# Optimization experiments

Measured on AMD Instinct MI355X. Metric: run time of the kernel, lower is better.

The kernel has to match this reference:

```python
import jax, jax.numpy as jnp
import numpy as np

D_MODEL = 512
N_HEADS = 8
D_HEAD = D_MODEL // N_HEADS


def setup_inputs() -> dict:
    key = jax.random.key(0)
    ks = jax.random.split(key, 10)
    B, N = 4, 2048
    s = 1.0 / np.sqrt(D_MODEL)
    inp = {
        'x': jax.random.normal(ks[0], (B, N, D_MODEL), jnp.float32),
        'attn_bias': jax.random.normal(ks[1], (B, 1, N, N), jnp.float32),
        'wq': jax.random.normal(ks[2], (D_MODEL, D_MODEL), jnp.float32) * s,
        'bq': jnp.zeros((D_MODEL,), jnp.float32),
        'wk': jax.random.normal(ks[3], (D_MODEL, D_MODEL), jnp.float32) * s,
        'bk': jnp.zeros((D_MODEL,), jnp.float32),
        'wv': jax.random.normal(ks[4], (D_MODEL, D_MODEL), jnp.float32) * s,
        'bv': jnp.zeros((D_MODEL,), jnp.float32),
        'wo': jax.random.normal(ks[5], (D_MODEL, D_MODEL), jnp.float32) * s,
        'bo': jnp.zeros((D_MODEL,), jnp.float32),
    }
    return inp


def reference(x, attn_bias, wq, bq, wk, bk, wv, bv, wo, bo):
    B, N, D = x.shape
    h, dh = N_HEADS, D_HEAD
    # projections; weights stored as (in, out) so y = x @ w + b
    q = (x @ wq + bq).reshape(B, N, h, dh).transpose(0, 2, 1, 3)  # (B,h,N,dh)
    k = (x @ wk + bk).reshape(B, N, h, dh).transpose(0, 2, 1, 3)
    v = (x @ wv + bv).reshape(B, N, h, dh).transpose(0, 2, 1, 3)
    scores = jnp.einsum('bhnd,bhmd->bhnm', q, k) / jnp.sqrt(jnp.float32(dh))
    scores = scores + attn_bias  # broadcast over heads
    attn = jax.nn.softmax(scores, axis=-1)
    out = jnp.einsum('bhnm,bhmd->bhnd', attn, v)
    out = out.transpose(0, 2, 1, 3).reshape(B, N, D)
    return out @ wo + bo
```

## Files before the change

kernel.cpp:

```cpp
#include <hip/hip_runtime.h>
#include <hip/hip_bf16.h>

typedef __bf16 bf16x8 __attribute__((ext_vector_type(8)));
typedef float f32x4 __attribute__((ext_vector_type(4)));
typedef float f32x16 __attribute__((ext_vector_type(16)));
using u16 = unsigned short;
using u32 = unsigned int;

#define LDSS 72

__device__ __forceinline__ u16 f2bf(float f) {
  union { float f; u32 u; } v; v.f = f;
  u32 r = v.u + 0x7fffu + ((v.u >> 16) & 1u);
  return (u16)(r >> 16);
}

__device__ __forceinline__ u32 cvt_pk_bf16(float lo, float hi) {
  u32 r;
  asm("v_cvt_pk_bf16_f32 %0, %1, %2" : "=v"(r) : "v"(lo), "v"(hi));
  return r;
}

__global__ void cast_x_kernel(const float* __restrict__ x, u16* __restrict__ xb) {
  int i = (blockIdx.x * 256 + threadIdx.x) * 8;
  float4 f0 = *(const float4*)&x[i];
  float4 f1 = *(const float4*)&x[i + 4];
  u16 u[8];
  u[0] = f2bf(f0.x); u[1] = f2bf(f0.y); u[2] = f2bf(f0.z); u[3] = f2bf(f0.w);
  u[4] = f2bf(f1.x); u[5] = f2bf(f1.y); u[6] = f2bf(f1.z); u[7] = f2bf(f1.w);
  *(uint4*)&xb[i] = *(uint4*)u;
}

__global__ __launch_bounds__(256) void cast_wT_kernel(
    const float* __restrict__ w0, const float* __restrict__ w1,
    const float* __restrict__ w2, const float* __restrict__ w3,
    u16* __restrict__ t0, u16* __restrict__ t1,
    u16* __restrict__ t2, u16* __restrict__ t3) {
  __shared__ u16 tl[64][72];
  int wi = blockIdx.z;
  const float* w; u16* t;
  if (wi == 0)      { w = w0; t = t0; }
  else if (wi == 1) { w = w1; t = t1; }
  else if (wi == 2) { w = w2; t = t2; }
  else              { w = w3; t = t3; }
  int r0 = blockIdx.x * 64, c0 = blockIdx.y * 64;
  int tid = threadIdx.x;
  int row = tid >> 2, q = tid & 3;
#pragma unroll
  for (int j = 0; j < 4; j++) {
    float4 f = *(const float4*)&w[(r0 + row) * 512 + c0 + q * 16 + j * 4];
    tl[row][q * 16 + j * 4 + 0] = f2bf(f.x);
    tl[row][q * 16 + j * 4 + 1] = f2bf(f.y);
    tl[row][q * 16 + j * 4 + 2] = f2bf(f.z);
    tl[row][q * 16 + j * 4 + 3] = f2bf(f.w);
  }
  __syncthreads();
  int crow = tid >> 2;
  u16 tmp[16];
#pragma unroll
  for (int j = 0; j < 16; j++) tmp[j] = tl[q * 16 + j][crow];
  *(uint4*)&t[(c0 + crow) * 512 + r0 + q * 16]     = *(uint4*)&tmp[0];
  *(uint4*)&t[(c0 + crow) * 512 + r0 + q * 16 + 8] = *(uint4*)&tmp[8];
}

__global__ __launch_bounds__(256) void proj_kernel(
    const u16* __restrict__ xb,
    const u16* __restrict__ wqT, const u16* __restrict__ wkT, const u16* __restrict__ wvT,
    const float* __restrict__ bq, const float* __restrict__ bk, const float* __restrict__ bv,
    u16* __restrict__ Q, u16* __restrict__ K, u16* __restrict__ Vt) {
  __shared__ u16 Alds[64 * LDSS];
  __shared__ u16 Blds[64 * LDSS];
  int which = blockIdx.z;
  const u16* wT; const float* bias; u16* out;
  if (which == 0)      { wT = wqT; bias = bq; out = Q; }
  else if (which == 1) { wT = wkT; bias = bk; out = K; }
  else                 { wT = wvT; bias = bv; out = Vt; }

  int m0 = blockIdx.y * 64;
  int n0 = blockIdx.x * 64;
  int tid = threadIdx.x;
  int lane = tid & 63, w = tid >> 6;
  int wm = w >> 1, wn = w & 1;
  int l15 = lane & 15, l4 = lane >> 4;

  int r0 = tid >> 3, c8 = (tid & 7) * 8;

  uint4 ar0 = *(const uint4*)&xb[(m0 + r0) * 512 + c8];
  uint4 ar1 = *(const uint4*)&xb[(m0 + r0 + 32) * 512 + c8];
  uint4 br0 = *(const uint4*)&wT[(n0 + r0) * 512 + c8];
  uint4 br1 = *(const uint4*)&wT[(n0 + r0 + 32) * 512 + c8];

  f32x4 acc[2][2] = {};
  for (int ks = 0; ks < 8; ks++) {
    __syncthreads();
    *(uint4*)&Alds[r0 * LDSS + c8]        = ar0;
    *(uint4*)&Alds[(r0 + 32) * LDSS + c8] = ar1;
    *(uint4*)&Blds[r0 * LDSS + c8]        = br0;
    *(uint4*)&Blds[(r0 + 32) * LDSS + c8] = br1;
    __syncthreads();
    if (ks < 7) {
      int k0 = (ks + 1) * 64;
      ar0 = *(const uint4*)&xb[(m0 + r0) * 512 + k0 + c8];
      ar1 = *(const uint4*)&xb[(m0 + r0 + 32) * 512 + k0 + c8];
      br0 = *(const uint4*)&wT[(n0 + r0) * 512 + k0 + c8];
      br1 = *(const uint4*)&wT[(n0 + r0 + 32) * 512 + k0 + c8];
    }
#pragma unroll
    for (int kk = 0; kk < 2; kk++) {
      bf16x8 a[2], b[2];
#pragma unroll
      for (int f = 0; f < 2; f++) {
        a[f] = *(const bf16x8*)&Alds[(wm * 32 + f * 16 + l15) * LDSS + kk * 32 + l4 * 8];
        b[f] = *(const bf16x8*)&Blds[(wn * 32 + f * 16 + l15) * LDSS + kk * 32 + l4 * 8];
      }
#pragma unroll
      for (int fm = 0; fm < 2; fm++)
#pragma unroll
        for (int fn = 0; fn < 2; fn++) {
          if (which == 2)
            acc[fm][fn] = __builtin_amdgcn_mfma_f32_16x16x32_bf16(b[fn], a[fm], acc[fm][fn], 0, 0, 0);
          else
            acc[fm][fn] = __builtin_amdgcn_mfma_f32_16x16x32_bf16(a[fm], b[fn], acc[fm][fn], 0, 0, 0);
        }
    }
  }
  int bidx = m0 >> 11;
  int head = n0 >> 6;
  if (which == 2) {
#pragma unroll
    for (int fm = 0; fm < 2; fm++)
#pragma unroll
      for (int fn = 0; fn < 2; fn++)
#pragma unroll
        for (int r = 0; r < 4; r++) {
          int drow = wn * 32 + fn * 16 + l4 * 4 + r;
          int col  = wm * 32 + fm * 16 + l15;
          float vv = acc[fm][fn][r] + bias[n0 + drow];
          out[((size_t)(bidx * 8 + head) * 64 + drow) * 2048 + (m0 & 2047) + col] = f2bf(vv);
        }
  } else {
#pragma unroll
    for (int fm = 0; fm < 2; fm++)
#pragma unroll
      for (int fn = 0; fn < 2; fn++)
#pragma unroll
        for (int r = 0; r < 4; r++) {
          int row = wm * 32 + fm * 16 + l4 * 4 + r;
          int col = wn * 32 + fn * 16 + l15;
          int nrow = (m0 & 2047) + row;
          float vv = acc[fm][fn][r] + bias[n0 + col];
          out[(((size_t)(bidx * 8 + head) * 2048) + nrow) * 64 + col] = f2bf(vv);
        }
  }
}

__global__ __launch_bounds__(256, 2) void attn_kernel(
    const u16* __restrict__ Q, const u16* __restrict__ K, const u16* __restrict__ Vt,
    const float* __restrict__ bias, u16* __restrict__ O) {
  __shared__ u16 Klds[64 * LDSS];
  __shared__ u16 Vtlds[64 * LDSS];

  int qt = blockIdx.x, h = blockIdx.y, b = blockIdx.z;
  int tid = threadIdx.x;
  int lane = tid & 63, w = tid >> 6;
  int l31 = lane & 31, hi = lane >> 5;
  int qrow = qt * 128 + w * 32 + l31;

  const u16* Qbh  = Q  + (size_t)(b * 8 + h) * 2048 * 64;
  const u16* Kbh  = K  + (size_t)(b * 8 + h) * 2048 * 64;
  const u16* Vtbh = Vt + (size_t)(b * 8 + h) * 64 * 2048;
  const float* biasq = bias + (size_t)b * 2048 * 2048 + (size_t)qrow * 2048;

  bf16x8 qf[4];
#pragma unroll
  for (int dk = 0; dk < 4; dk++)
    qf[dk] = *(const bf16x8*)&Qbh[qrow * 64 + dk * 16 + hi * 8];

  f32x16 o[2] = {};
  float mrow = -1e30f, lrow = 0.f;

  int r0 = tid >> 3, c8 = (tid & 7) * 8;

  uint4 kr0 = *(const uint4*)&Kbh[r0 * 64 + c8];
  uint4 kr1 = *(const uint4*)&Kbh[(32 + r0) * 64 + c8];
  uint4 vr0 = *(const uint4*)&Vtbh[r0 * 2048 + c8];
  uint4 vr1 = *(const uint4*)&Vtbh[(r0 + 32) * 2048 + c8];
  float4 bb[8];
#pragma unroll
  for (int kt = 0; kt < 2; kt++)
#pragma unroll
    for (int g = 0; g < 4; g++)
      bb[kt * 4 + g] = *(const float4*)&biasq[kt * 32 + 8 * g + 4 * hi];

  for (int t = 0; t < 32; t++) {
    __syncthreads();
    *(uint4*)&Klds[r0 * LDSS + c8]         = kr0;
    *(uint4*)&Klds[(r0 + 32) * LDSS + c8]  = kr1;
    *(uint4*)&Vtlds[r0 * LDSS + c8]        = vr0;
    *(uint4*)&Vtlds[(r0 + 32) * LDSS + c8] = vr1;
    __syncthreads();

    bool pf = (t < 31);
    if (pf) {
      kr0 = *(const uint4*)&Kbh[((t + 1) * 64 + r0) * 64 + c8];
      kr1 = *(const uint4*)&Kbh[((t + 1) * 64 + 32 + r0) * 64 + c8];
      vr0 = *(const uint4*)&Vtbh[r0 * 2048 + (t + 1) * 64 + c8];
      vr1 = *(const uint4*)&Vtbh[(r0 + 32) * 2048 + (t + 1) * 64 + c8];
    }

    f32x16 s[2] = {};
    __builtin_amdgcn_s_setprio(1);
#pragma unroll
    for (int dk = 0; dk < 4; dk++) {
      bf16x8 a0 = *(const bf16x8*)&Klds[l31 * LDSS + dk * 16 + hi * 8];
      s[0] = __builtin_amdgcn_mfma_f32_32x32x16_bf16(a0, qf[dk], s[0], 0, 0, 0);
      bf16x8 a1 = *(const bf16x8*)&Klds[(32 + l31) * LDSS + dk * 16 + hi * 8];
      s[1] = __builtin_amdgcn_mfma_f32_32x32x16_bf16(a1, qf[dk], s[1], 0, 0, 0);
    }
    __builtin_amdgcn_s_setprio(0);

    float m = -1e30f;
#pragma unroll
    for (int kt = 0; kt < 2; kt++)
#pragma unroll
      for (int g = 0; g < 4; g++) {
        float4 bv4 = bb[kt * 4 + g];
#pragma unroll
        for (int j = 0; j < 4; j++) {
          float val = s[kt][g * 4 + j] * 0.125f + ((const float*)&bv4)[j];
          s[kt][g * 4 + j] = val;
          m = fmaxf(m, val);
        }
      }
    m = fmaxf(m, __shfl_xor(m, 32));

    if (!__all(m <= mrow + 8.0f)) {
      float mnew = fmaxf(mrow, m);
      float corr = __expf(mrow - mnew);
      mrow = mnew;
      lrow *= corr;
#pragma unroll
      for (int dt = 0; dt < 2; dt++)
#pragma unroll
        for (int i = 0; i < 16; i++) o[dt][i] *= corr;
    }

    u32 c[2][8];
    float sum = 0.f;
#pragma unroll
    for (int kt = 0; kt < 2; kt++)
#pragma unroll
      for (int g = 0; g < 4; g++) {
        float p0 = __expf(s[kt][g * 4 + 0] - mrow);
        float p1 = __expf(s[kt][g * 4 + 1] - mrow);
        float p2 = __expf(s[kt][g * 4 + 2] - mrow);
        float p3 = __expf(s[kt][g * 4 + 3] - mrow);
        sum += (p0 + p1) + (p2 + p3);
        c[kt][2 * g]     = cvt_pk_bf16(p0, p1);
        c[kt][2 * g + 1] = cvt_pk_bf16(p2, p3);
      }
    sum += __shfl_xor(sum, 32);
    lrow += sum;

    u32 dx[2][8];
#pragma unroll
    for (int kt = 0; kt < 2; kt++)
#pragma unroll
      for (int j = 0; j < 8; j++)
        dx[kt][j] = (u32)__shfl_xor((int)c[kt][j], 32);

    if (pf) {
#pragma unroll
      for (int kt = 0; kt < 2; kt++)
#pragma unroll
        for (int g = 0; g < 4; g++)
          bb[kt * 4 + g] = *(const float4*)&biasq[(t + 1) * 64 + kt * 32 + 8 * g + 4 * hi];
    }

    __builtin_amdgcn_s_setprio(1);
#pragma unroll
    for (int kk = 0; kk < 4; kk++) {
      const int kt = kk >> 1, jA = 4 * (kk & 1);
      union { u32 u[4]; bf16x8 v; } pfg;
      pfg.u[0] = hi ? dx[kt][jA + 2] : c[kt][jA];
      pfg.u[1] = hi ? dx[kt][jA + 3] : c[kt][jA + 1];
      pfg.u[2] = hi ? c[kt][jA + 2]  : dx[kt][jA];
      pfg.u[3] = hi ? c[kt][jA + 3]  : dx[kt][jA + 1];
#pragma unroll
      for (int dt = 0; dt < 2; dt++) {
        bf16x8 va = *(const bf16x8*)&Vtlds[(dt * 32 + l31) * LDSS + kk * 16 + hi * 8];
        o[dt] = __builtin_amdgcn_mfma_f32_32x32x16_bf16(va, pfg.v, o[dt], 0, 0, 0);
      }
    }
    __builtin_amdgcn_s_setprio(0);
  }

  float inv = 1.0f / lrow;
  size_t obase = (size_t)(b * 2048 + qrow) * 512 + h * 64;
#pragma unroll
  for (int dt = 0; dt < 2; dt++)
#pragma unroll
    for (int g = 0; g < 4; g++) {
      uint2 pr;
      pr.x = cvt_pk_bf16(o[dt][4 * g + 0] * inv, o[dt][4 * g + 1] * inv);
      pr.y = cvt_pk_bf16(o[dt][4 * g + 2] * inv, o[dt][4 * g + 3] * inv);
      *(uint2*)&O[obase + dt * 32 + 8 * g + 4 * hi] = pr;
    }
}

__global__ __launch_bounds__(256) void outproj_kernel(
    const u16* __restrict__ Ob, const u16* __restrict__ woT,
    const float* __restrict__ bo, float* __restrict__ out) {
  __shared__ u16 Alds[64 * LDSS];
  __shared__ u16 Blds[64 * LDSS];
  int m0 = blockIdx.y * 64;
  int n0 = blockIdx.x * 64;
  int tid = threadIdx.x;
  int lane = tid & 63, w = tid >> 6;
  int wm = w >> 1, wn = w & 1;
  int l15 = lane & 15, l4 = lane >> 4;

  int r0 = tid >> 3, c8 = (tid & 7) * 8;
  uint4 ar0 = *(const uint4*)&Ob[(m0 + r0) * 512 + c8];
  uint4 ar1 = *(const uint4*)&Ob[(m0 + r0 + 32) * 512 + c8];
  uint4 br0 = *(const uint4*)&woT[(n0 + r0) * 512 + c8];
  uint4 br1 = *(const uint4*)&woT[(n0 + r0 + 32) * 512 + c8];

  f32x4 acc[2][2] = {};
  for (int ks = 0; ks < 8; ks++) {
    __syncthreads();
    *(uint4*)&Alds[r0 * LDSS + c8]        = ar0;
    *(uint4*)&Alds[(r0 + 32) * LDSS + c8] = ar1;
    *(uint4*)&Blds[r0 * LDSS + c8]        = br0;
    *(uint4*)&Blds[(r0 + 32) * LDSS + c8] = br1;
    __syncthreads();
    if (ks < 7) {
      int k0 = (ks + 1) * 64;
      ar0 = *(const uint4*)&Ob[(m0 + r0) * 512 + k0 + c8];
      ar1 = *(const uint4*)&Ob[(m0 + r0 + 32) * 512 + k0 + c8];
      br0 = *(const uint4*)&woT[(n0 + r0) * 512 + k0 + c8];
      br1 = *(const uint4*)&woT[(n0 + r0 + 32) * 512 + k0 + c8];
    }
#pragma unroll
    for (int kk = 0; kk < 2; kk++) {
      bf16x8 a[2], bfr[2];
#pragma unroll
      for (int f = 0; f < 2; f++) {
        a[f] = *(const bf16x8*)&Alds[(wm * 32 + f * 16 + l15) * LDSS + kk * 32 + l4 * 8];
        bfr[f] = *(const bf16x8*)&Blds[(wn * 32 + f * 16 + l15) * LDSS + kk * 32 + l4 * 8];
      }
#pragma unroll
      for (int fm = 0; fm < 2; fm++)
#pragma unroll
        for (int fn = 0; fn < 2; fn++)
          acc[fm][fn] = __builtin_amdgcn_mfma_f32_16x16x32_bf16(a[fm], bfr[fn], acc[fm][fn], 0, 0, 0);
    }
  }
#pragma unroll
  for (int fm = 0; fm < 2; fm++)
#pragma unroll
    for (int fn = 0; fn < 2; fn++)
#pragma unroll
      for (int r = 0; r < 4; r++) {
        int row = wm * 32 + fm * 16 + l4 * 4 + r;
        int col = wn * 32 + fn * 16 + l15;
        out[(size_t)(m0 + row) * 512 + n0 + col] = acc[fm][fn][r] + bo[n0 + col];
      }
}

extern "C" void kernel_launch(void* const* d_in, const int* in_sizes, int n_in,
                              void* d_out, int out_size, void* d_ws, size_t ws_size,
                              hipStream_t stream) {
  const float* x    = (const float*)d_in[0];
  const float* bias = (const float*)d_in[1];
  const float* wq   = (const float*)d_in[2];
  const float* bq   = (const float*)d_in[3];
  const float* wk   = (const float*)d_in[4];
  const float* bk   = (const float*)d_in[5];
  const float* wv   = (const float*)d_in[6];
  const float* bv   = (const float*)d_in[7];
  const float* wo   = (const float*)d_in[8];
  const float* bo   = (const float*)d_in[9];
  float* out = (float*)d_out;

  char* ws = (char*)d_ws;
  u16* xb  = (u16*)(ws + 0);
  u16* wqT = (u16*)(ws + 8388608);
  u16* wkT = (u16*)(ws + 8912896);
  u16* wvT = (u16*)(ws + 9437184);
  u16* woT = (u16*)(ws + 9961472);
  u16* Qb  = (u16*)(ws + 10485760);
  u16* Kb  = (u16*)(ws + 18874368);
  u16* VtB = (u16*)(ws + 27262976);
  u16* Ob  = (u16*)(ws + 35651584);

  hipLaunchKernelGGL(cast_x_kernel, dim3(2048), dim3(256), 0, stream, x, xb);
  hipLaunchKernelGGL(cast_wT_kernel, dim3(8, 8, 4), dim3(256), 0, stream,
                     wq, wk, wv, wo, wqT, wkT, wvT, woT);
  hipLaunchKernelGGL(proj_kernel, dim3(8, 128, 3), dim3(256), 0, stream,
                     xb, wqT, wkT, wvT, bq, bk, bv, Qb, Kb, VtB);
  hipLaunchKernelGGL(attn_kernel, dim3(16, 8, 4), dim3(256), 0, stream,
                     Qb, Kb, VtB, bias, Ob);
  hipLaunchKernelGGL(outproj_kernel, dim3(8, 128), dim3(256), 0, stream,
                     Ob, woT, bo, out);
}
```

Measured before the change: 135.2 us.

## Split attention over key range into two halves and merge partial softmax

Adds a split-K (flash-decoding style) attention path. Each block processes 16 of 32 key tiles, grid doubles to 1024 blocks, and it writes fp32 partial outputs plus per-row max and sum. A merge kernel then combines the two halves into bf16 output. The goal is more parallelism to fill the 256 CUs, since the original 512 blocks at 2 per CU underfill the GPU. The cost is extra fp32 partial traffic (about 32 MB each way), one more launch, and a fallback when workspace is too small.

```diff
diff --git a/kernel.cpp b/kernel.cpp
--- a/kernel.cpp
+++ b/kernel.cpp
@@ -154,13 +154,15 @@
   }
 }
 
-__global__ __launch_bounds__(256, 2) void attn_kernel(
+template <int SPLIT>
+__device__ __forceinline__ void attn_body(
     const u16* __restrict__ Q, const u16* __restrict__ K, const u16* __restrict__ Vt,
-    const float* __restrict__ bias, u16* __restrict__ O) {
+    const float* __restrict__ bias, u16* __restrict__ O,
+    float* __restrict__ Opart, float2* __restrict__ mlb,
+    int qt, int h, int b, int s, int tbase, int TILES) {
   __shared__ u16 Klds[64 * LDSS];
   __shared__ u16 Vtlds[64 * LDSS];
 
-  int qt = blockIdx.x, h = blockIdx.y, b = blockIdx.z;
   int tid = threadIdx.x;
   int lane = tid & 63, w = tid >> 6;
   int l31 = lane & 31, hi = lane >> 5;
@@ -181,18 +183,19 @@
 
   int r0 = tid >> 3, c8 = (tid & 7) * 8;
 
-  uint4 kr0 = *(const uint4*)&Kbh[r0 * 64 + c8];
-  uint4 kr1 = *(const uint4*)&Kbh[(32 + r0) * 64 + c8];
-  uint4 vr0 = *(const uint4*)&Vtbh[r0 * 2048 + c8];
-  uint4 vr1 = *(const uint4*)&Vtbh[(r0 + 32) * 2048 + c8];
+  uint4 kr0 = *(const uint4*)&Kbh[(tbase * 64 + r0) * 64 + c8];
+  uint4 kr1 = *(const uint4*)&Kbh[(tbase * 64 + 32 + r0) * 64 + c8];
+  uint4 vr0 = *(const uint4*)&Vtbh[r0 * 2048 + tbase * 64 + c8];
+  uint4 vr1 = *(const uint4*)&Vtbh[(r0 + 32) * 2048 + tbase * 64 + c8];
   float4 bb[8];
 #pragma unroll
   for (int kt = 0; kt < 2; kt++)
 #pragma unroll
     for (int g = 0; g < 4; g++)
-      bb[kt * 4 + g] = *(const float4*)&biasq[kt * 32 + 8 * g + 4 * hi];
-
-  for (int t = 0; t < 32; t++) {
+      bb[kt * 4 + g] = *(const float4*)&biasq[tbase * 64 + kt * 32 + 8 * g + 4 * hi];
+
+  for (int t = 0; t < TILES; t++) {
+    int tile = tbase + t;
     __syncthreads();
     *(uint4*)&Klds[r0 * LDSS + c8]         = kr0;
     *(uint4*)&Klds[(r0 + 32) * LDSS + c8]  = kr1;
@@ -200,22 +203,22 @@
     *(uint4*)&Vtlds[(r0 + 32) * LDSS + c8] = vr1;
     __syncthreads();
 
-    bool pf = (t < 31);
+    bool pf = (t < TILES - 1);
     if (pf) {
-      kr0 = *(const uint4*)&Kbh[((t + 1) * 64 + r0) * 64 + c8];
-      kr1 = *(const uint4*)&Kbh[((t + 1) * 64 + 32 + r0) * 64 + c8];
-      vr0 = *(const uint4*)&Vtbh[r0 * 2048 + (t + 1) * 64 + c8];
-      vr1 = *(const uint4*)&Vtbh[(r0 + 32) * 2048 + (t + 1) * 64 + c8];
-    }
-
-    f32x16 s[2] = {};
+      kr0 = *(const uint4*)&Kbh[((tile + 1) * 64 + r0) * 64 + c8];
+      kr1 = *(const uint4*)&Kbh[((tile + 1) * 64 + 32 + r0) * 64 + c8];
+      vr0 = *(const uint4*)&Vtbh[r0 * 2048 + (tile + 1) * 64 + c8];
+      vr1 = *(const uint4*)&Vtbh[(r0 + 32) * 2048 + (tile + 1) * 64 + c8];
+    }
+
+    f32x16 sR[2] = {};
     __builtin_amdgcn_s_setprio(1);
 #pragma unroll
     for (int dk = 0; dk < 4; dk++) {
       bf16x8 a0 = *(const bf16x8*)&Klds[l31 * LDSS + dk * 16 + hi * 8];
-      s[0] = __builtin_amdgcn_mfma_f32_32x32x16_bf16(a0, qf[dk], s[0], 0, 0, 0);
+      sR[0] = __builtin_amdgcn_mfma_f32_32x32x16_bf16(a0, qf[dk], sR[0], 0, 0, 0);
       bf16x8 a1 = *(const bf16x8*)&Klds[(32 + l31) * LDSS + dk * 16 + hi * 8];
-      s[1] = __builtin_amdgcn_mfma_f32_32x32x16_bf16(a1, qf[dk], s[1], 0, 0, 0);
+      sR[1] = __builtin_amdgcn_mfma_f32_32x32x16_bf16(a1, qf[dk], sR[1], 0, 0, 0);
     }
     __builtin_amdgcn_s_setprio(0);
 
@@ -227,8 +230,8 @@
         float4 bv4 = bb[kt * 4 + g];
 #pragma unroll
         for (int j = 0; j < 4; j++) {
-          float val = s[kt][g * 4 + j] * 0.125f + ((const float*)&bv4)[j];
-          s[kt][g * 4 + j] = val;
+          float val = sR[kt][g * 4 + j] * 0.125f + ((const float*)&bv4)[j];
+          sR[kt][g * 4 + j] = val;
           m = fmaxf(m, val);
         }
       }
@@ -251,10 +254,10 @@
     for (int kt = 0; kt < 2; kt++)
 #pragma unroll
       for (int g = 0; g < 4; g++) {
-        float p0 = __expf(s[kt][g * 4 + 0] - mrow);
-        float p1 = __expf(s[kt][g * 4 + 1] - mrow);
-        float p2 = __expf(s[kt][g * 4 + 2] - mrow);
-        float p3 = __expf(s[kt][g * 4 + 3] - mrow);
+        float p0 = __expf(sR[kt][g * 4 + 0] - mrow);
+        float p1 = __expf(sR[kt][g * 4 + 1] - mrow);
+        float p2 = __expf(sR[kt][g * 4 + 2] - mrow);
+        float p3 = __expf(sR[kt][g * 4 + 3] - mrow);
         sum += (p0 + p1) + (p2 + p3);
         c[kt][2 * g]     = cvt_pk_bf16(p0, p1);
         c[kt][2 * g + 1] = cvt_pk_bf16(p2, p3);
@@ -274,7 +277,7 @@
       for (int kt = 0; kt < 2; kt++)
 #pragma unroll
         for (int g = 0; g < 4; g++)
-          bb[kt * 4 + g] = *(const float4*)&biasq[(t + 1) * 64 + kt * 32 + 8 * g + 4 * hi];
+          bb[kt * 4 + g] = *(const float4*)&biasq[(tile + 1) * 64 + kt * 32 + 8 * g + 4 * hi];
     }
 
     __builtin_amdgcn_s_setprio(1);
@@ -295,17 +298,72 @@
     __builtin_amdgcn_s_setprio(0);
   }
 
-  float inv = 1.0f / lrow;
-  size_t obase = (size_t)(b * 2048 + qrow) * 512 + h * 64;
-#pragma unroll
-  for (int dt = 0; dt < 2; dt++)
-#pragma unroll
-    for (int g = 0; g < 4; g++) {
-      uint2 pr;
-      pr.x = cvt_pk_bf16(o[dt][4 * g + 0] * inv, o[dt][4 * g + 1] * inv);
-      pr.y = cvt_pk_bf16(o[dt][4 * g + 2] * inv, o[dt][4 * g + 3] * inv);
-      *(uint2*)&O[obase + dt * 32 + 8 * g + 4 * hi] = pr;
-    }
+  if (SPLIT == 0) {
+    float inv = 1.0f / lrow;
+    size_t obase = (size_t)(b * 2048 + qrow) * 512 + h * 64;
+#pragma unroll
+    for (int dt = 0; dt < 2; dt++)
+#pragma unroll
+      for (int g = 0; g < 4; g++) {
+        uint2 pr;
+        pr.x = cvt_pk_bf16(o[dt][4 * g + 0] * inv, o[dt][4 * g + 1] * inv);
+        pr.y = cvt_pk_bf16(o[dt][4 * g + 2] * inv, o[dt][4 * g + 3] * inv);
+        *(uint2*)&O[obase + dt * 32 + 8 * g + 4 * hi] = pr;
+      }
+  } else {
+    float* P = Opart + (size_t)s * (4 * 2048 * 512) + (size_t)(b * 2048 + qrow) * 512 + h * 64;
+#pragma unroll
+    for (int dt = 0; dt < 2; dt++)
+#pragma unroll
+      for (int g = 0; g < 4; g++)
+        *(float4*)&P[dt * 32 + 8 * g + 4 * hi] =
+            make_float4(o[dt][4 * g + 0], o[dt][4 * g + 1], o[dt][4 * g + 2], o[dt][4 * g + 3]);
+    if (hi == 0)
+      mlb[(size_t)s * (4 * 8 * 2048) + (size_t)(b * 8 + h) * 2048 + qrow] = make_float2(mrow, lrow);
+  }
+}
+
+__global__ __launch_bounds__(256, 2) void attn_kernel(
+    const u16* __restrict__ Q, const u16* __restrict__ K, const u16* __restrict__ Vt,
+    const float* __restrict__ bias, u16* __restrict__ O) {
+  attn_body<0>(Q, K, Vt, bias, O, nullptr, nullptr,
+               blockIdx.x, blockIdx.y, blockIdx.z, 0, 0, 32);
+}
+
+__global__ __launch_bounds__(256, 2) void attn_split_kernel(
+    const u16* __restrict__ Q, const u16* __restrict__ K, const u16* __restrict__ Vt,
+    const float* __restrict__ bias, float* __restrict__ Opart, float2* __restrict__ mlb) {
+  int z = blockIdx.z;
+  int b = z >> 1, s = z & 1;
+  attn_body<1>(Q, K, Vt, bias, nullptr, Opart, mlb,
+               blockIdx.x, blockIdx.y, b, s, s * 16, 16);
+}
+
+__global__ __launch_bounds__(256) void merge_kernel(
+    const float* __restrict__ Opart, const float2* __restrict__ mlb,
+    u16* __restrict__ Ob) {
+  int i = blockIdx.x * 256 + threadIdx.x;
+  size_t e = (size_t)i * 8;
+  int row = (int)(e >> 9);
+  int col = (int)(e & 511);
+  int b = row >> 11, q = row & 2047;
+  int h = col >> 6;
+  float2 ml0 = mlb[(size_t)(b * 8 + h) * 2048 + q];
+  float2 ml1 = mlb[(size_t)(4 * 8 * 2048) + (size_t)(b * 8 + h) * 2048 + q];
+  float M = fmaxf(ml0.x, ml1.x);
+  float w0 = __expf(ml0.x - M), w1 = __expf(ml1.x - M);
+  float inv = 1.0f / (ml0.y * w0 + ml1.y * w1);
+  w0 *= inv; w1 *= inv;
+  float4 a0 = *(const float4*)&Opart[e];
+  float4 a1 = *(const float4*)&Opart[e + 4];
+  float4 b0 = *(const float4*)&Opart[(size_t)(4 * 2048 * 512) + e];
+  float4 b1 = *(const float4*)&Opart[(size_t)(4 * 2048 * 512) + e + 4];
+  u16 r[8];
+  r[0] = f2bf(a0.x * w0 + b0.x * w1); r[1] = f2bf(a0.y * w0 + b0.y * w1);
+  r[2] = f2bf(a0.z * w0 + b0.z * w1); r[3] = f2bf(a0.w * w0 + b0.w * w1);
+  r[4] = f2bf(a1.x * w0 + b1.x * w1); r[5] = f2bf(a1.y * w0 + b1.y * w1);
+  r[6] = f2bf(a1.z * w0 + b1.z * w1); r[7] = f2bf(a1.w * w0 + b1.w * w1);
+  *(uint4*)&Ob[e] = *(uint4*)r;
 }
 
 __global__ __launch_bounds__(256) void outproj_kernel(
@@ -393,14 +451,24 @@
   u16* Kb  = (u16*)(ws + 18874368);
   u16* VtB = (u16*)(ws + 27262976);
   u16* Ob  = (u16*)(ws + 35651584);
+  float*  Opart = (float*)(ws + 44040192);
+  float2* mlb   = (float2*)(ws + 77594624);
+  const size_t NEED = 78643200ULL;
 
   hipLaunchKernelGGL(cast_x_kernel, dim3(2048), dim3(256), 0, stream, x, xb);
   hipLaunchKernelGGL(cast_wT_kernel, dim3(8, 8, 4), dim3(256), 0, stream,
                      wq, wk, wv, wo, wqT, wkT, wvT, woT);
   hipLaunchKernelGGL(proj_kernel, dim3(8, 128, 3), dim3(256), 0, stream,
                      xb, wqT, wkT, wvT, bq, bk, bv, Qb, Kb, VtB);
-  hipLaunchKernelGGL(attn_kernel, dim3(16, 8, 4), dim3(256), 0, stream,
-                     Qb, Kb, VtB, bias, Ob);
+  if (ws_size >= NEED) {
+    hipLaunchKernelGGL(attn_split_kernel, dim3(16, 8, 8), dim3(256), 0, stream,
+                       Qb, Kb, VtB, bias, Opart, mlb);
+    hipLaunchKernelGGL(merge_kernel, dim3(2048), dim3(256), 0, stream,
+                       Opart, mlb, Ob);
+  } else {
+    hipLaunchKernelGGL(attn_kernel, dim3(16, 8, 4), dim3(256), 0, stream,
+                       Qb, Kb, VtB, bias, Ob);
+  }
   hipLaunchKernelGGL(outproj_kernel, dim3(8, 128), dim3(256), 0, stream,
                      Ob, woT, bo, out);
 }
```

Measured after the change: 145.6 us. 7.7% more time.
